# Kernel tuning notes

Measured on AMD Instinct MI355X. Metric: run time of the kernel, lower is better.

## Reference

```python
import jax, jax.numpy as jnp
import numpy as np

N_NODES = 50000
N_EDGES = 800000
N_GRAPHS = 64
IN_CH = 64
HID = 64


def _gcn(x, W, b, src, dst, norm, self_norm, n):
    # GCNConv with self-loops and symmetric normalization (PyG defaults)
    h = x @ W  # [N, H]
    agg = jax.ops.segment_sum(norm[:, None] * h[src], dst, num_segments=n)
    return agg + self_norm[:, None] * h + b


def setup_inputs() -> dict:
    key = jax.random.key(0)
    ks = jax.random.split(key, 20)
    s = 0.1
    d = {
        'x': jax.random.normal(ks[0], (N_NODES, IN_CH), jnp.float32),
        'x_SC': jax.random.normal(ks[1], (N_NODES, IN_CH), jnp.float32),
        'W1': jax.random.normal(ks[2], (IN_CH, HID), jnp.float32) * s,
        'b1': jax.random.normal(ks[3], (HID,), jnp.float32) * s,
        'W2': jax.random.normal(ks[4], (HID, HID), jnp.float32) * s,
        'b2': jax.random.normal(ks[5], (HID,), jnp.float32) * s,
        'We': jax.random.normal(ks[6], (IN_CH, HID), jnp.float32) * s,
        'be': jax.random.normal(ks[7], (HID,), jnp.float32) * s,
        'W1s': jax.random.normal(ks[8], (IN_CH, HID), jnp.float32) * s,
        'b1s': jax.random.normal(ks[9], (HID,), jnp.float32) * s,
        'W2s': jax.random.normal(ks[10], (HID, HID), jnp.float32) * s,
        'b2s': jax.random.normal(ks[11], (HID,), jnp.float32) * s,
        'Wes': jax.random.normal(ks[12], (IN_CH, HID), jnp.float32) * s,
        'bes': jax.random.normal(ks[13], (HID,), jnp.float32) * s,
        'Wf': jax.random.normal(ks[14], (HID, 1), jnp.float32) * s,
        'bf': jax.random.normal(ks[15], (1,), jnp.float32) * s,
        'edge_index': jax.random.randint(ks[16], (2, N_EDGES), 0, N_NODES, jnp.int32),
        'batch': jnp.sort(jax.random.randint(ks[17], (N_NODES,), 0, N_GRAPHS, jnp.int32)),
        'num_graphs': N_GRAPHS,
    }
    return d


def reference(x, x_SC, W1, b1, W2, b2, We, be, W1s, b1s, W2s, b2s, Wes, bes, Wf, bf, edge_index, batch, num_graphs):
    n = x.shape[0]
    src, dst = edge_index[0], edge_index[1]
    # degree with self-loops (edge weight 1)
    deg = jnp.ones((n,), x.dtype).at[dst].add(jnp.ones((src.shape[0],), x.dtype))
    dinv = deg ** -0.5
    norm = dinv[src] * dinv[dst]
    self_norm = dinv * dinv

    h = jax.nn.relu(_gcn(x, W1, b1, src, dst, norm, self_norm, n)) + jax.nn.relu(x @ We + be)
    h = jax.nn.relu(_gcn(h, W2, b2, src, dst, norm, self_norm, n)) + h

    hs = jax.nn.relu(_gcn(x_SC, W1s, b1s, src, dst, norm, self_norm, n)) + jax.nn.relu(x_SC @ Wes + bes)
    hs = jax.nn.relu(_gcn(hs, W2s, b2s, src, dst, norm, self_norm, n)) + hs

    h = h + hs
    sums = jax.ops.segment_sum(h, batch, num_segments=num_graphs)
    cnts = jax.ops.segment_sum(jnp.ones((n,), h.dtype), batch, num_segments=num_graphs)
    pooled = sums / jnp.maximum(cnts, 1.0)[:, None]
    return pooled @ Wf + bf
```

## Files before the change

kernel.cpp:

```cpp
#include <hip/hip_runtime.h>
#include <stdint.h>


typedef _Float16 f16;
typedef _Float16 f16x2 __attribute__((ext_vector_type(2)));
typedef _Float16 f16x8 __attribute__((ext_vector_type(8)));
typedef float f32x4 __attribute__((ext_vector_type(4)));

__global__ void deg_count_k(const int* __restrict__ dst, int nE, int* __restrict__ cnt) {
    int i = blockIdx.x * blockDim.x + threadIdx.x;
    if (i < nE) atomicAdd(&cnt[dst[i]], 1);
}

__global__ void dinv_k(const int* __restrict__ cnt, int n, float* __restrict__ dinv) {
    int i = blockIdx.x * blockDim.x + threadIdx.x;
    if (i < n) dinv[i] = 1.0f / sqrtf(1.0f + (float)cnt[i]);
}

__global__ __launch_bounds__(256) void scanA_k(const int* __restrict__ cnt, int n,
                                               int* __restrict__ offs, int* __restrict__ bsums) {
    int tid = threadIdx.x, lane = tid & 63, wid = tid >> 6;
    int base = blockIdx.x * 1024 + tid * 4;
    int v0 = (base + 0 < n) ? cnt[base + 0] : 0;
    int v1 = (base + 1 < n) ? cnt[base + 1] : 0;
    int v2 = (base + 2 < n) ? cnt[base + 2] : 0;
    int v3 = (base + 3 < n) ? cnt[base + 3] : 0;
    int lsum = v0 + v1 + v2 + v3;
    int s = lsum;
#pragma unroll
    for (int off = 1; off < 64; off <<= 1) {
        int t = __shfl_up(s, off);
        if (lane >= off) s += t;
    }
    __shared__ int wt[4];
    if (lane == 63) wt[wid] = s;
    __syncthreads();
    int woff = 0;
    for (int w = 0; w < wid; ++w) woff += wt[w];
    int excl = woff + s - lsum;
    if (base + 0 < n) offs[base + 0] = excl;
    if (base + 1 < n) offs[base + 1] = excl + v0;
    if (base + 2 < n) offs[base + 2] = excl + v0 + v1;
    if (base + 3 < n) offs[base + 3] = excl + v0 + v1 + v2;
    if (tid == 0) bsums[blockIdx.x] = wt[0] + wt[1] + wt[2] + wt[3];
}

__global__ void scanB_k(const int* __restrict__ bsums, int nb, int* __restrict__ boffs) {
    int lane = threadIdx.x;
    int carry = 0;
    for (int base = 0; base < nb; base += 64) {
        int i = base + lane;
        int v = (i < nb) ? bsums[i] : 0;
        int s = v;
#pragma unroll
        for (int off = 1; off < 64; off <<= 1) {
            int t = __shfl_up(s, off);
            if (lane >= off) s += t;
        }
        if (i < nb) boffs[i] = carry + s - v;
        carry += __shfl(s, 63);
    }
}

__global__ __launch_bounds__(256) void scanC_k(int* __restrict__ offs,
                                               const int* __restrict__ boffs,
                                               int* __restrict__ cur, int n, int nE) {
    int boff = boffs[blockIdx.x];
    int base = blockIdx.x * 1024 + threadIdx.x * 4;
#pragma unroll
    for (int j = 0; j < 4; ++j) {
        int i = base + j;
        if (i < n) {
            int o = offs[i] + boff;
            offs[i] = o;
            cur[i] = o;
        }
    }
    if (blockIdx.x == 0 && threadIdx.x == 0) offs[n] = nE;
}

__global__ void fill_k(const int* __restrict__ src, const int* __restrict__ dst, int nE,
                       int* __restrict__ cur, int* __restrict__ elist) {
    int e = blockIdx.x * blockDim.x + threadIdx.x;
    if (e < nE) {
        int p = atomicAdd(&cur[dst[e]], 1);
        elist[p] = src[e];
    }
}

template <int NW, bool F16IN>
__global__ __launch_bounds__(256) void mm_mfma_k(
    const void* __restrict__ X1, const void* __restrict__ X2,
    const float* __restrict__ Wa1, const float* __restrict__ Wa2,
    const float* __restrict__ Wc1, const float* __restrict__ Wc2,
    const float* __restrict__ dinv,
    f16* __restrict__ Oa1, f16* __restrict__ Oa2,
    f16* __restrict__ Oc1, f16* __restrict__ Oc2,
    int xP, int oP, int n) {
    const int branch = blockIdx.y;
    const void* X   = branch ? X2 : X1;
    const float* Wa = branch ? Wa2 : Wa1;
    const float* Wc = branch ? Wc2 : Wc1;
    f16* Oa = branch ? Oa2 : Oa1;
    f16* Oc = branch ? Oc2 : Oc1;

    const int lane = threadIdx.x & 63;
    const int col = lane & 15;
    const int kgrp = lane >> 4;

    f16x8 wa[4][2], wc[4][2];
#pragma unroll
    for (int ct = 0; ct < 4; ++ct)
#pragma unroll
        for (int kk = 0; kk < 2; ++kk) {
#pragma unroll
            for (int j = 0; j < 8; ++j) {
                int widx = (kk * 32 + kgrp * 8 + j) * 64 + ct * 16 + col;
                wa[ct][kk][j] = (f16)Wa[widx];
                if (NW == 2) wc[ct][kk][j] = (f16)Wc[widx];
            }
        }

    const int wid = blockIdx.x * 4 + (threadIdx.x >> 6);
    const int nwaves = gridDim.x * 4;
    const int ntiles = (n + 15) >> 4;
    for (int t = wid; t < ntiles; t += nwaves) {
        int arow = t * 16 + col;
        if (arow >= n) arow = n - 1;
        f16x8 af[2];
#pragma unroll
        for (int kk = 0; kk < 2; ++kk) {
            if (F16IN) {
                af[kk] = *(const f16x8*)((const f16*)X + (size_t)arow * xP + kk * 32 + kgrp * 8);
            } else {
                const float4* px = (const float4*)((const float*)X + (size_t)arow * xP + kk * 32 + kgrp * 8);
                float4 u0 = px[0], u1 = px[1];
                af[kk][0] = (f16)u0.x; af[kk][1] = (f16)u0.y;
                af[kk][2] = (f16)u0.z; af[kk][3] = (f16)u0.w;
                af[kk][4] = (f16)u1.x; af[kk][5] = (f16)u1.y;
                af[kk][6] = (f16)u1.z; af[kk][7] = (f16)u1.w;
            }
        }
        f32x4 acca[4], accc[4];
#pragma unroll
        for (int ct = 0; ct < 4; ++ct) {
            acca[ct] = (f32x4)(0.0f);
            if (NW == 2) accc[ct] = (f32x4)(0.0f);
        }
#pragma unroll
        for (int ct = 0; ct < 4; ++ct)
#pragma unroll
            for (int kk = 0; kk < 2; ++kk) {
                acca[ct] = __builtin_amdgcn_mfma_f32_16x16x32_f16(af[kk], wa[ct][kk], acca[ct], 0, 0, 0);
                if (NW == 2)
                    accc[ct] = __builtin_amdgcn_mfma_f32_16x16x32_f16(af[kk], wc[ct][kk], accc[ct], 0, 0, 0);
            }
        int rbase = t * 16 + kgrp * 4;
#pragma unroll
        for (int j = 0; j < 4; ++j) {
            int row = rbase + j;
            if (row < n) {
                float d = dinv[row];
#pragma unroll
                for (int ct = 0; ct < 4; ++ct) {
                    Oa[(size_t)row * oP + ct * 16 + col] = (f16)(d * acca[ct][j]);
                    if (NW == 2)
                        Oc[(size_t)row * oP + ct * 16 + col] = (f16)(accc[ct][j]);
                }
            }
        }
    }
}

__global__ __launch_bounds__(256) void agg1_k(
    const int* __restrict__ offs, const int* __restrict__ elist,
    const uint32_t* __restrict__ Aw, const uint32_t* __restrict__ Sw,
    const float* __restrict__ b1, const float* __restrict__ b1s,
    const float* __restrict__ be, const float* __restrict__ bes,
    const float* __restrict__ dinv, uint32_t* __restrict__ Hw, int n) {
    int node = blockIdx.x * 4 + (threadIdx.x >> 6);
    int lane = threadIdx.x & 63;
    if (node >= n) return;
    int br = lane >> 5;
    int ch0 = (lane & 31) * 2;
    float bb0 = br ? b1s[ch0] : b1[ch0];
    float bb1 = br ? b1s[ch0 + 1] : b1[ch0 + 1];
    float bs0 = br ? bes[ch0] : be[ch0];
    float bs1 = br ? bes[ch0 + 1] : be[ch0 + 1];

    int e0 = offs[node], e1 = offs[node + 1];
    f16x2 selfv = __builtin_bit_cast(f16x2, Aw[(size_t)node * 64 + lane]);
    float acc0 = (float)selfv.x, acc1 = (float)selfv.y;
    int e = e0;
    for (; e + 7 < e1; e += 8) {
        int s0 = elist[e], s1 = elist[e + 1], s2 = elist[e + 2], s3 = elist[e + 3];
        int s4 = elist[e + 4], s5 = elist[e + 5], s6 = elist[e + 6], s7 = elist[e + 7];
        f16x2 v0 = __builtin_bit_cast(f16x2, Aw[(size_t)s0 * 64 + lane]);
        f16x2 v1 = __builtin_bit_cast(f16x2, Aw[(size_t)s1 * 64 + lane]);
        f16x2 v2 = __builtin_bit_cast(f16x2, Aw[(size_t)s2 * 64 + lane]);
        f16x2 v3 = __builtin_bit_cast(f16x2, Aw[(size_t)s3 * 64 + lane]);
        f16x2 v4 = __builtin_bit_cast(f16x2, Aw[(size_t)s4 * 64 + lane]);
        f16x2 v5 = __builtin_bit_cast(f16x2, Aw[(size_t)s5 * 64 + lane]);
        f16x2 v6 = __builtin_bit_cast(f16x2, Aw[(size_t)s6 * 64 + lane]);
        f16x2 v7 = __builtin_bit_cast(f16x2, Aw[(size_t)s7 * 64 + lane]);
        acc0 += (((float)v0.x + (float)v1.x) + ((float)v2.x + (float)v3.x)) +
                (((float)v4.x + (float)v5.x) + ((float)v6.x + (float)v7.x));
        acc1 += (((float)v0.y + (float)v1.y) + ((float)v2.y + (float)v3.y)) +
                (((float)v4.y + (float)v5.y) + ((float)v6.y + (float)v7.y));
    }
    for (; e < e1; ++e) {
        f16x2 v = __builtin_bit_cast(f16x2, Aw[(size_t)elist[e] * 64 + lane]);
        acc0 += (float)v.x;
        acc1 += (float)v.y;
    }
    float d = dinv[node];
    float g0 = fmaxf(d * acc0 + bb0, 0.0f);
    float g1 = fmaxf(d * acc1 + bb1, 0.0f);
    f16x2 sv = __builtin_bit_cast(f16x2, Sw[(size_t)node * 64 + lane]);
    g0 += fmaxf((float)sv.x + bs0, 0.0f);
    g1 += fmaxf((float)sv.y + bs1, 0.0f);
    f16x2 o; o.x = (f16)g0; o.y = (f16)g1;
    Hw[(size_t)node * 64 + lane] = __builtin_bit_cast(uint32_t, o);
}

__global__ __launch_bounds__(256) void agg2_dot_k(
    const int* __restrict__ offs, const int* __restrict__ elist,
    const uint32_t* __restrict__ Aw, const uint32_t* __restrict__ Hw,
    const float* __restrict__ b2, const float* __restrict__ b2s,
    const float* __restrict__ Wf, const float* __restrict__ dinv,
    float* __restrict__ dot, int n) {
    int node = blockIdx.x * 4 + (threadIdx.x >> 6);
    int lane = threadIdx.x & 63;
    if (node >= n) return;
    int br = lane >> 5;
    int ch0 = (lane & 31) * 2;
    float bb0 = br ? b2s[ch0] : b2[ch0];
    float bb1 = br ? b2s[ch0 + 1] : b2[ch0 + 1];
    float wf0 = Wf[ch0], wf1 = Wf[ch0 + 1];

    int e0 = offs[node], e1 = offs[node + 1];
    f16x2 selfv = __builtin_bit_cast(f16x2, Aw[(size_t)node * 64 + lane]);
    float acc0 = (float)selfv.x, acc1 = (float)selfv.y;
    int e = e0;
    for (; e + 7 < e1; e += 8) {
        int s0 = elist[e], s1 = elist[e + 1], s2 = elist[e + 2], s3 = elist[e + 3];
        int s4 = elist[e + 4], s5 = elist[e + 5], s6 = elist[e + 6], s7 = elist[e + 7];
        f16x2 v0 = __builtin_bit_cast(f16x2, Aw[(size_t)s0 * 64 + lane]);
        f16x2 v1 = __builtin_bit_cast(f16x2, Aw[(size_t)s1 * 64 + lane]);
        f16x2 v2 = __builtin_bit_cast(f16x2, Aw[(size_t)s2 * 64 + lane]);
        f16x2 v3 = __builtin_bit_cast(f16x2, Aw[(size_t)s3 * 64 + lane]);
        f16x2 v4 = __builtin_bit_cast(f16x2, Aw[(size_t)s4 * 64 + lane]);
        f16x2 v5 = __builtin_bit_cast(f16x2, Aw[(size_t)s5 * 64 + lane]);
        f16x2 v6 = __builtin_bit_cast(f16x2, Aw[(size_t)s6 * 64 + lane]);
        f16x2 v7 = __builtin_bit_cast(f16x2, Aw[(size_t)s7 * 64 + lane]);
        acc0 += (((float)v0.x + (float)v1.x) + ((float)v2.x + (float)v3.x)) +
                (((float)v4.x + (float)v5.x) + ((float)v6.x + (float)v7.x));
        acc1 += (((float)v0.y + (float)v1.y) + ((float)v2.y + (float)v3.y)) +
                (((float)v4.y + (float)v5.y) + ((float)v6.y + (float)v7.y));
    }
    for (; e < e1; ++e) {
        f16x2 v = __builtin_bit_cast(f16x2, Aw[(size_t)elist[e] * 64 + lane]);
        acc0 += (float)v.x;
        acc1 += (float)v.y;
    }
    float d = dinv[node];
    f16x2 hv = __builtin_bit_cast(f16x2, Hw[(size_t)node * 64 + lane]);
    float h0 = fmaxf(d * acc0 + bb0, 0.0f) + (float)hv.x;
    float h1 = fmaxf(d * acc1 + bb1, 0.0f) + (float)hv.y;
    float c = h0 * wf0 + h1 * wf1;
#pragma unroll
    for (int off = 32; off > 0; off >>= 1) c += __shfl_down(c, off);
    if (lane == 0) dot[node] = c;
}

__device__ inline int lower_bound(const int* __restrict__ batch, int n, int g) {
    int lo = 0, hi = n;
    while (lo < hi) {
        int mid = (lo + hi) >> 1;
        if (batch[mid] < g) lo = mid + 1; else hi = mid;
    }
    return lo;
}

__global__ __launch_bounds__(256) void pool_reduce_k(
    const float* __restrict__ dot, const int* __restrict__ batch, int n,
    const float* __restrict__ bf, float* __restrict__ out) {
    int g = blockIdx.x;
    int start = lower_bound(batch, n, g);
    int end = lower_bound(batch, n, g + 1);
    int tid = threadIdx.x, lane = tid & 63, wid = tid >> 6;
    float acc = 0.f;
    for (int i = start + tid; i < end; i += blockDim.x) acc += dot[i];
#pragma unroll
    for (int off = 32; off > 0; off >>= 1) acc += __shfl_down(acc, off);
    __shared__ float part[4];
    if (lane == 0) part[wid] = acc;
    __syncthreads();
    if (tid == 0) {
        float s = part[0] + part[1] + part[2] + part[3];
        float cnt = fmaxf((float)(end - start), 1.0f);
        out[g] = s / cnt + bf[0];
    }
}

static inline char* alignp(char* p, uintptr_t a) {
    return (char*)(((uintptr_t)p + a - 1) & ~(a - 1));
}

extern "C" void kernel_launch(void* const* d_in, const int* in_sizes, int n_in,
                              void* d_out, int out_size, void* d_ws, size_t ws_size,
                              hipStream_t stream) {
    const float* x    = (const float*)d_in[0];
    const float* x_SC = (const float*)d_in[1];
    const float* W1   = (const float*)d_in[2];
    const float* b1   = (const float*)d_in[3];
    const float* W2   = (const float*)d_in[4];
    const float* b2   = (const float*)d_in[5];
    const float* We   = (const float*)d_in[6];
    const float* be   = (const float*)d_in[7];
    const float* W1s  = (const float*)d_in[8];
    const float* b1s  = (const float*)d_in[9];
    const float* W2s  = (const float*)d_in[10];
    const float* b2s  = (const float*)d_in[11];
    const float* Wes  = (const float*)d_in[12];
    const float* bes  = (const float*)d_in[13];
    const float* Wf   = (const float*)d_in[14];
    const float* bf   = (const float*)d_in[15];
    const int* ei     = (const int*)d_in[16];
    const int* batch  = (const int*)d_in[17];

    const int nN = in_sizes[0] / 64;
    const int nE = in_sizes[16] / 2;
    const int nG = out_size;
    const int* esrc = ei;
    const int* edst = ei + nE;
    const int nb = (nN + 1023) / 1024;

    char* p = (char*)d_ws;
    int* cur    = (int*)p;   p = alignp(p + (size_t)nN * sizeof(int), 64);
    int* offs   = (int*)p;   p = alignp(p + (size_t)(nN + 1) * sizeof(int), 64);
    int* elist  = (int*)p;   p = alignp(p + (size_t)nE * sizeof(int), 64);
    int* bsums  = (int*)p;   p = alignp(p + 1024 * sizeof(int), 64);
    int* boffs  = (int*)p;   p = alignp(p + 1024 * sizeof(int), 64);
    float* dinv = (float*)p; p = alignp(p + (size_t)nN * sizeof(float), 64);
    float* dot  = (float*)p; p = alignp(p + (size_t)nN * sizeof(float), 64);
    f16* A = (f16*)p;        p = alignp(p + (size_t)nN * 128 * sizeof(f16), 64);
    f16* S = (f16*)p;        p = alignp(p + (size_t)nN * 128 * sizeof(f16), 64);
    f16* H = (f16*)p;        p = alignp(p + (size_t)nN * 128 * sizeof(f16), 64);

    const int thr = 256;
    const int gEdgeT = (nE + thr - 1) / thr;
    const int gNodeT = (nN + thr - 1) / thr;
    const int gNodeW = (nN + 3) / 4;

    hipMemsetAsync(cur, 0, (size_t)nN * sizeof(int), stream);
    deg_count_k<<<gEdgeT, thr, 0, stream>>>(edst, nE, cur);
    dinv_k<<<gNodeT, thr, 0, stream>>>(cur, nN, dinv);
    scanA_k<<<nb, thr, 0, stream>>>(cur, nN, offs, bsums);
    scanB_k<<<1, 64, 0, stream>>>(bsums, nb, boffs);
    scanC_k<<<nb, thr, 0, stream>>>(offs, boffs, cur, nN, nE);
    fill_k<<<gEdgeT, thr, 0, stream>>>(esrc, edst, nE, cur, elist);

    mm_mfma_k<2, false><<<dim3(256, 2), thr, 0, stream>>>(
        x, x_SC, W1, W1s, We, Wes, dinv,
        A, A + 64, S, S + 64, 64, 128, nN);
    agg1_k<<<gNodeW, thr, 0, stream>>>(offs, elist, (const uint32_t*)A, (const uint32_t*)S,
                                       b1, b1s, be, bes, dinv, (uint32_t*)H, nN);

    mm_mfma_k<1, true><<<dim3(256, 2), thr, 0, stream>>>(
        H, H + 64, W2, W2s, nullptr, nullptr, dinv,
        A, A + 64, nullptr, nullptr, 128, 128, nN);
    agg2_dot_k<<<gNodeW, thr, 0, stream>>>(offs, elist, (const uint32_t*)A, (const uint32_t*)H,
                                           b2, b2s, Wf, dinv, dot, nN);

    pool_reduce_k<<<nG, thr, 0, stream>>>(dot, batch, nN, bf, (float*)d_out);
}
```

Measured before the change: 319.3 us.

## Record atomic ranks during degree count to drop second atomic pass and kernels

```diff
diff --git a/kernel.cpp b/kernel.cpp
--- a/kernel.cpp
+++ b/kernel.cpp
@@ -7,24 +7,25 @@
 typedef _Float16 f16x8 __attribute__((ext_vector_type(8)));
 typedef float f32x4 __attribute__((ext_vector_type(4)));
 
-__global__ void deg_count_k(const int* __restrict__ dst, int nE, int* __restrict__ cnt) {
+__global__ void deg_rank_k(const int* __restrict__ dst, int nE,
+                           int* __restrict__ cnt, int* __restrict__ rank_) {
     int i = blockIdx.x * blockDim.x + threadIdx.x;
-    if (i < nE) atomicAdd(&cnt[dst[i]], 1);
-}
-
-__global__ void dinv_k(const int* __restrict__ cnt, int n, float* __restrict__ dinv) {
-    int i = blockIdx.x * blockDim.x + threadIdx.x;
-    if (i < n) dinv[i] = 1.0f / sqrtf(1.0f + (float)cnt[i]);
+    if (i < nE) rank_[i] = atomicAdd(&cnt[dst[i]], 1);
 }
 
 __global__ __launch_bounds__(256) void scanA_k(const int* __restrict__ cnt, int n,
-                                               int* __restrict__ offs, int* __restrict__ bsums) {
+                                               int* __restrict__ offs, int* __restrict__ bsums,
+                                               float* __restrict__ dinv) {
     int tid = threadIdx.x, lane = tid & 63, wid = tid >> 6;
     int base = blockIdx.x * 1024 + tid * 4;
     int v0 = (base + 0 < n) ? cnt[base + 0] : 0;
     int v1 = (base + 1 < n) ? cnt[base + 1] : 0;
     int v2 = (base + 2 < n) ? cnt[base + 2] : 0;
     int v3 = (base + 3 < n) ? cnt[base + 3] : 0;
+    if (base + 0 < n) dinv[base + 0] = 1.0f / sqrtf(1.0f + (float)v0);
+    if (base + 1 < n) dinv[base + 1] = 1.0f / sqrtf(1.0f + (float)v1);
+    if (base + 2 < n) dinv[base + 2] = 1.0f / sqrtf(1.0f + (float)v2);
+    if (base + 3 < n) dinv[base + 3] = 1.0f / sqrtf(1.0f + (float)v3);
     int lsum = v0 + v1 + v2 + v3;
     int s = lsum;
 #pragma unroll
@@ -45,47 +46,25 @@
     if (tid == 0) bsums[blockIdx.x] = wt[0] + wt[1] + wt[2] + wt[3];
 }
 
-__global__ void scanB_k(const int* __restrict__ bsums, int nb, int* __restrict__ boffs) {
-    int lane = threadIdx.x;
-    int carry = 0;
-    for (int base = 0; base < nb; base += 64) {
-        int i = base + lane;
-        int v = (i < nb) ? bsums[i] : 0;
-        int s = v;
-#pragma unroll
-        for (int off = 1; off < 64; off <<= 1) {
-            int t = __shfl_up(s, off);
-            if (lane >= off) s += t;
-        }
-        if (i < nb) boffs[i] = carry + s - v;
-        carry += __shfl(s, 63);
-    }
-}
-
 __global__ __launch_bounds__(256) void scanC_k(int* __restrict__ offs,
-                                               const int* __restrict__ boffs,
-                                               int* __restrict__ cur, int n, int nE) {
-    int boff = boffs[blockIdx.x];
+                                               const int* __restrict__ bsums,
+                                               int n, int nE) {
+    int boff = 0;
+    for (int b = 0; b < (int)blockIdx.x; ++b) boff += bsums[b];
     int base = blockIdx.x * 1024 + threadIdx.x * 4;
 #pragma unroll
     for (int j = 0; j < 4; ++j) {
         int i = base + j;
-        if (i < n) {
-            int o = offs[i] + boff;
-            offs[i] = o;
-            cur[i] = o;
-        }
+        if (i < n) offs[i] += boff;
     }
     if (blockIdx.x == 0 && threadIdx.x == 0) offs[n] = nE;
 }
 
-__global__ void fill_k(const int* __restrict__ src, const int* __restrict__ dst, int nE,
-                       int* __restrict__ cur, int* __restrict__ elist) {
+__global__ void fill_rank_k(const int* __restrict__ src, const int* __restrict__ dst,
+                            const int* __restrict__ rank_, const int* __restrict__ offs,
+                            int* __restrict__ elist, int nE) {
     int e = blockIdx.x * blockDim.x + threadIdx.x;
-    if (e < nE) {
-        int p = atomicAdd(&cur[dst[e]], 1);
-        elist[p] = src[e];
-    }
+    if (e < nE) elist[offs[dst[e]] + rank_[e]] = src[e];
 }
 
 template <int NW, bool F16IN>
@@ -337,11 +316,11 @@
     const int nb = (nN + 1023) / 1024;
 
     char* p = (char*)d_ws;
-    int* cur    = (int*)p;   p = alignp(p + (size_t)nN * sizeof(int), 64);
+    int* cnt    = (int*)p;   p = alignp(p + (size_t)nN * sizeof(int), 64);
+    int* rank_  = (int*)p;   p = alignp(p + (size_t)nE * sizeof(int), 64);
     int* offs   = (int*)p;   p = alignp(p + (size_t)(nN + 1) * sizeof(int), 64);
+    int* bsums  = (int*)p;   p = alignp(p + 1024 * sizeof(int), 64);
     int* elist  = (int*)p;   p = alignp(p + (size_t)nE * sizeof(int), 64);
-    int* bsums  = (int*)p;   p = alignp(p + 1024 * sizeof(int), 64);
-    int* boffs  = (int*)p;   p = alignp(p + 1024 * sizeof(int), 64);
     float* dinv = (float*)p; p = alignp(p + (size_t)nN * sizeof(float), 64);
     float* dot  = (float*)p; p = alignp(p + (size_t)nN * sizeof(float), 64);
     f16* A = (f16*)p;        p = alignp(p + (size_t)nN * 128 * sizeof(f16), 64);
@@ -350,16 +329,13 @@
 
     const int thr = 256;
     const int gEdgeT = (nE + thr - 1) / thr;
-    const int gNodeT = (nN + thr - 1) / thr;
     const int gNodeW = (nN + 3) / 4;
 
-    hipMemsetAsync(cur, 0, (size_t)nN * sizeof(int), stream);
-    deg_count_k<<<gEdgeT, thr, 0, stream>>>(edst, nE, cur);
-    dinv_k<<<gNodeT, thr, 0, stream>>>(cur, nN, dinv);
-    scanA_k<<<nb, thr, 0, stream>>>(cur, nN, offs, bsums);
-    scanB_k<<<1, 64, 0, stream>>>(bsums, nb, boffs);
-    scanC_k<<<nb, thr, 0, stream>>>(offs, boffs, cur, nN, nE);
-    fill_k<<<gEdgeT, thr, 0, stream>>>(esrc, edst, nE, cur, elist);
+    hipMemsetAsync(cnt, 0, (size_t)nN * sizeof(int), stream);
+    deg_rank_k<<<gEdgeT, thr, 0, stream>>>(edst, nE, cnt, rank_);
+    scanA_k<<<nb, thr, 0, stream>>>(cnt, nN, offs, bsums, dinv);
+    scanC_k<<<nb, thr, 0, stream>>>(offs, bsums, nN, nE);
+    fill_rank_k<<<gEdgeT, thr, 0, stream>>>(esrc, edst, rank_, offs, elist, nE);
 
     mm_mfma_k<2, false><<<dim3(256, 2), thr, 0, stream>>>(
         x, x_SC, W1, W1s, We, Wes, dinv,
```

Result: faster. 280.5 us (-12.1%).
